# Optimization experiments

Hardware: AMD Instinct MI355X
Metric: run time of the kernel (lower is better)

The kernel has to match this reference:

```python
import jax, jax.numpy as jnp
import numpy as np

TEMPERATURE = 0.3


def setup_inputs() -> dict:
    key = jax.random.key(0)
    k1, k2, k3 = jax.random.split(key, 3)
    B, C = 65536, 1000
    logits = jax.random.normal(k1, (B, C), dtype=jnp.float32)
    targets = jax.random.randint(k2, (B,), 0, C, dtype=jnp.int64)
    similarity_matrix = jax.random.uniform(k3, (C, C), dtype=jnp.float32)
    return {"logits": logits, "targets": targets, "similarity_matrix": similarity_matrix}


def reference(logits, targets, similarity_matrix):
    # Gather per-sample similarity rows: [B, C]
    sim_rows = similarity_matrix[targets]
    # soft_targets = normalized exp(-sim/T) == softmax(-sim/T) along classes
    soft_targets = jax.nn.softmax(-sim_rows / TEMPERATURE, axis=1)
    log_probs = jax.nn.log_softmax(logits, axis=1)
    loss = -(soft_targets * log_probs).sum(axis=1).mean()
    return loss
```

## Files before the change

### kernel.cpp

```cpp
#include <hip/hip_runtime.h>
#include <math.h>


#define TEMPERATURE 0.3f
#define C_DIM 1000
#define LOSS_BLOCKS 2048

typedef float f4 __attribute__((ext_vector_type(4)));

__device__ __forceinline__ float waveAllSum(float v) {
    #pragma unroll
    for (int m = 1; m < 64; m <<= 1) v += __shfl_xor(v, m, 64);
    return v;
}

__global__ void soft_targets_kernel(const float* __restrict__ sim,
                                    float* __restrict__ P) {
    const int wid  = threadIdx.x >> 6;
    const int lane = threadIdx.x & 63;
    const int c = blockIdx.x * 4 + wid;

    const f4* row  = (const f4*)(sim + (size_t)c * C_DIM);
    f4*       prow = (f4*)(P + (size_t)c * C_DIM);

    const bool tail = lane < 58;
    const int  i3   = tail ? lane + 192 : lane;

    f4 v0 = row[lane];
    f4 v1 = row[lane + 64];
    f4 v2 = row[lane + 128];
    f4 v3 = row[i3];

    const float s = -1.0f / TEMPERATURE;
    f4 e0, e1, e2, e3;
    e0.x = __expf(v0.x * s); e0.y = __expf(v0.y * s); e0.z = __expf(v0.z * s); e0.w = __expf(v0.w * s);
    e1.x = __expf(v1.x * s); e1.y = __expf(v1.y * s); e1.z = __expf(v1.z * s); e1.w = __expf(v1.w * s);
    e2.x = __expf(v2.x * s); e2.y = __expf(v2.y * s); e2.z = __expf(v2.z * s); e2.w = __expf(v2.w * s);
    e3.x = __expf(v3.x * s); e3.y = __expf(v3.y * s); e3.z = __expf(v3.z * s); e3.w = __expf(v3.w * s);

    float sum = (e0.x + e0.y + e0.z + e0.w)
              + (e1.x + e1.y + e1.z + e1.w)
              + (e2.x + e2.y + e2.z + e2.w)
              + (tail ? (e3.x + e3.y + e3.z + e3.w) : 0.0f);
    sum = waveAllSum(sum);
    const float inv = 1.0f / sum;

    prow[lane]       = e0 * inv;
    prow[lane + 64]  = e1 * inv;
    prow[lane + 128] = e2 * inv;
    if (tail) prow[lane + 192] = e3 * inv;
}

__device__ __forceinline__ void sample_body(const float* __restrict__ logits,
                                            const float* __restrict__ P,
                                            int i, int t, int lane, int i3, bool tail,
                                            float& es_out, float& acc_dt) {
    const f4* lrow = (const f4*)(logits + (size_t)i * C_DIM);
    const f4* prow = (const f4*)(P + (size_t)t * C_DIM);

    f4 a0 = __builtin_nontemporal_load(lrow + lane);
    f4 a1 = __builtin_nontemporal_load(lrow + lane + 64);
    f4 a2 = __builtin_nontemporal_load(lrow + lane + 128);
    f4 a3 = __builtin_nontemporal_load(lrow + i3);
    f4 p0 = prow[lane];
    f4 p1 = prow[lane + 64];
    f4 p2 = prow[lane + 128];
    f4 p3 = prow[i3];

    float es = (__expf(a0.x) + __expf(a0.y) + __expf(a0.z) + __expf(a0.w))
             + (__expf(a1.x) + __expf(a1.y) + __expf(a1.z) + __expf(a1.w))
             + (__expf(a2.x) + __expf(a2.y) + __expf(a2.z) + __expf(a2.w));
    float es3 = __expf(a3.x) + __expf(a3.y) + __expf(a3.z) + __expf(a3.w);

    float dt = a0.x * p0.x + a0.y * p0.y + a0.z * p0.z + a0.w * p0.w
             + a1.x * p1.x + a1.y * p1.y + a1.z * p1.z + a1.w * p1.w
             + a2.x * p2.x + a2.y * p2.y + a2.z * p2.z + a2.w * p2.w;
    float dt3 = a3.x * p3.x + a3.y * p3.y + a3.z * p3.z + a3.w * p3.w;

    if (tail) { es += es3; dt += dt3; }
    es_out = es;
    acc_dt += dt;
}

__global__ void loss_kernel(const float* __restrict__ logits,
                            const int* __restrict__ targets,
                            const float* __restrict__ P,
                            float* __restrict__ out,
                            float invB, int B) {
    const int wid  = threadIdx.x >> 6;
    const int lane = threadIdx.x & 63;
    const int wave   = blockIdx.x * 4 + wid;
    const int nwaves = gridDim.x * 4;

    const bool tail = lane < 58;
    const int  i3   = tail ? lane + 192 : lane;

    float acc_log = 0.0f;
    float acc_dt  = 0.0f;

    int i = wave;
    for (; i + nwaves < B; i += 2 * nwaves) {
        const int ta = targets[i];
        const int tb = targets[i + nwaves];
        float esA, esB;
        sample_body(logits, P, i,          ta, lane, i3, tail, esA, acc_dt);
        sample_body(logits, P, i + nwaves, tb, lane, i3, tail, esB, acc_dt);
        esA = waveAllSum(esA);
        esB = waveAllSum(esB);
        acc_log += __logf(esA) + __logf(esB);
    }
    for (; i < B; i += nwaves) {
        const int t = targets[i];
        float es;
        sample_body(logits, P, i, t, lane, i3, tail, es, acc_dt);
        es = waveAllSum(es);
        acc_log += __logf(es);
    }

    const float dt_total = waveAllSum(acc_dt);
    __shared__ float sloc[4];
    if (lane == 0) sloc[wid] = acc_log - dt_total;
    __syncthreads();
    if (threadIdx.x == 0) {
        const float blk = sloc[0] + sloc[1] + sloc[2] + sloc[3];
        atomicAdd(out, blk * invB);
    }
}

extern "C" void kernel_launch(void* const* d_in, const int* in_sizes, int n_in,
                              void* d_out, int out_size, void* d_ws, size_t ws_size,
                              hipStream_t stream) {
    const float* logits  = (const float*)d_in[0];
    const int*   targets = (const int*)d_in[1];
    const float* sim     = (const float*)d_in[2];
    float* out = (float*)d_out;
    float* P   = (float*)d_ws;

    const int B = in_sizes[1];

    hipMemsetAsync(out, 0, sizeof(float), stream);
    soft_targets_kernel<<<250, 256, 0, stream>>>(sim, P);
    loss_kernel<<<LOSS_BLOCKS, 256, 0, stream>>>(logits, targets, P, out,
                                                 1.0f / (float)B, B);
}
```

Before: 350.6 us.

## Software-pipeline loss loop with double-buffered loads and drop memset launch

Restructures the loss kernel loop to process chunks of 8 samples per wave, with their target indices prefetched. Each sample's logits and soft-target row loads are issued one sample ahead into a double buffer, so memory latency overlaps with the exp/dot computation. The output zeroing moves from a separate hipMemsetAsync into the soft-targets kernel, removing one launch. The extra in-flight registers may lower occupancy.

```diff
diff --git a/kernel.cpp b/kernel.cpp
--- a/kernel.cpp
+++ b/kernel.cpp
@@ -5,6 +5,7 @@
 #define TEMPERATURE 0.3f
 #define C_DIM 1000
 #define LOSS_BLOCKS 2048
+#define CHUNK 8
 
 typedef float f4 __attribute__((ext_vector_type(4)));
 
@@ -15,7 +16,10 @@
 }
 
 __global__ void soft_targets_kernel(const float* __restrict__ sim,
-                                    float* __restrict__ P) {
+                                    float* __restrict__ P,
+                                    float* __restrict__ out) {
+    if (blockIdx.x == 0 && threadIdx.x == 0) out[0] = 0.0f;
+
     const int wid  = threadIdx.x >> 6;
     const int lane = threadIdx.x & 63;
     const int c = blockIdx.x * 4 + wid;
@@ -51,42 +55,45 @@
     if (tail) prow[lane + 192] = e3 * inv;
 }
 
-__device__ __forceinline__ void sample_body(const float* __restrict__ logits,
+__device__ __forceinline__ void issue_loads(const float* __restrict__ logits,
                                             const float* __restrict__ P,
-                                            int i, int t, int lane, int i3, bool tail,
-                                            float& es_out, float& acc_dt) {
+                                            int i, int t, int lane, int i3,
+                                            f4* A, f4* Pp) {
     const f4* lrow = (const f4*)(logits + (size_t)i * C_DIM);
     const f4* prow = (const f4*)(P + (size_t)t * C_DIM);
+    A[0]  = __builtin_nontemporal_load(lrow + lane);
+    A[1]  = __builtin_nontemporal_load(lrow + lane + 64);
+    A[2]  = __builtin_nontemporal_load(lrow + lane + 128);
+    A[3]  = __builtin_nontemporal_load(lrow + i3);
+    Pp[0] = prow[lane];
+    Pp[1] = prow[lane + 64];
+    Pp[2] = prow[lane + 128];
+    Pp[3] = prow[i3];
+}
 
-    f4 a0 = __builtin_nontemporal_load(lrow + lane);
-    f4 a1 = __builtin_nontemporal_load(lrow + lane + 64);
-    f4 a2 = __builtin_nontemporal_load(lrow + lane + 128);
-    f4 a3 = __builtin_nontemporal_load(lrow + i3);
-    f4 p0 = prow[lane];
-    f4 p1 = prow[lane + 64];
-    f4 p2 = prow[lane + 128];
-    f4 p3 = prow[i3];
+__device__ __forceinline__ void compute_sample(const f4* A, const f4* Pp, bool tail,
+                                               float& es_out, float& acc_dt) {
+    float es = (__expf(A[0].x) + __expf(A[0].y) + __expf(A[0].z) + __expf(A[0].w))
+             + (__expf(A[1].x) + __expf(A[1].y) + __expf(A[1].z) + __expf(A[1].w))
+             + (__expf(A[2].x) + __expf(A[2].y) + __expf(A[2].z) + __expf(A[2].w));
+    float es3 = __expf(A[3].x) + __expf(A[3].y) + __expf(A[3].z) + __expf(A[3].w);
 
-    float es = (__expf(a0.x) + __expf(a0.y) + __expf(a0.z) + __expf(a0.w))
-             + (__expf(a1.x) + __expf(a1.y) + __expf(a1.z) + __expf(a1.w))
-             + (__expf(a2.x) + __expf(a2.y) + __expf(a2.z) + __expf(a2.w));
-    float es3 = __expf(a3.x) + __expf(a3.y) + __expf(a3.z) + __expf(a3.w);
-
-    float dt = a0.x * p0.x + a0.y * p0.y + a0.z * p0.z + a0.w * p0.w
-             + a1.x * p1.x + a1.y * p1.y + a1.z * p1.z + a1.w * p1.w
-             + a2.x * p2.x + a2.y * p2.y + a2.z * p2.z + a2.w * p2.w;
-    float dt3 = a3.x * p3.x + a3.y * p3.y + a3.z * p3.z + a3.w * p3.w;
+    float dt = A[0].x * Pp[0].x + A[0].y * Pp[0].y + A[0].z * Pp[0].z + A[0].w * Pp[0].w
+             + A[1].x * Pp[1].x + A[1].y * Pp[1].y + A[1].z * Pp[1].z + A[1].w * Pp[1].w
+             + A[2].x * Pp[2].x + A[2].y * Pp[2].y + A[2].z * Pp[2].z + A[2].w * Pp[2].w;
+    float dt3 = A[3].x * Pp[3].x + A[3].y * Pp[3].y + A[3].z * Pp[3].z + A[3].w * Pp[3].w;
 
     if (tail) { es += es3; dt += dt3; }
     es_out = es;
     acc_dt += dt;
 }
 
-__global__ void loss_kernel(const float* __restrict__ logits,
-                            const int* __restrict__ targets,
-                            const float* __restrict__ P,
-                            float* __restrict__ out,
-                            float invB, int B) {
+__global__ void __launch_bounds__(256)
+loss_kernel(const float* __restrict__ logits,
+            const int* __restrict__ targets,
+            const float* __restrict__ P,
+            float* __restrict__ out,
+            float invB, int B) {
     const int wid  = threadIdx.x >> 6;
     const int lane = threadIdx.x & 63;
     const int wave   = blockIdx.x * 4 + wid;
@@ -98,21 +105,35 @@
     float acc_log = 0.0f;
     float acc_dt  = 0.0f;
 
-    int i = wave;
-    for (; i + nwaves < B; i += 2 * nwaves) {
-        const int ta = targets[i];
-        const int tb = targets[i + nwaves];
-        float esA, esB;
-        sample_body(logits, P, i,          ta, lane, i3, tail, esA, acc_dt);
-        sample_body(logits, P, i + nwaves, tb, lane, i3, tail, esB, acc_dt);
-        esA = waveAllSum(esA);
-        esB = waveAllSum(esB);
-        acc_log += __logf(esA) + __logf(esB);
+    const int chunk_stride = CHUNK * nwaves;
+    int base = wave;
+
+    for (; base + chunk_stride - nwaves < B; base += chunk_stride) {
+        int t[CHUNK];
+        #pragma unroll
+        for (int k = 0; k < CHUNK; k++) t[k] = targets[base + k * nwaves];
+
+        f4 A[2][4], Pp[2][4];
+        issue_loads(logits, P, base, t[0], lane, i3, A[0], Pp[0]);
+
+        #pragma unroll
+        for (int k = 0; k < CHUNK; k++) {
+            if (k + 1 < CHUNK) {
+                issue_loads(logits, P, base + (k + 1) * nwaves, t[k + 1],
+                            lane, i3, A[(k + 1) & 1], Pp[(k + 1) & 1]);
+            }
+            float es;
+            compute_sample(A[k & 1], Pp[k & 1], tail, es, acc_dt);
+            es = waveAllSum(es);
+            acc_log += __logf(es);
+        }
     }
-    for (; i < B; i += nwaves) {
+    for (int i = base; i < B; i += nwaves) {
         const int t = targets[i];
+        f4 A[4], Pp[4];
+        issue_loads(logits, P, i, t, lane, i3, A, Pp);
         float es;
-        sample_body(logits, P, i, t, lane, i3, tail, es, acc_dt);
+        compute_sample(A, Pp, tail, es, acc_dt);
         es = waveAllSum(es);
         acc_log += __logf(es);
     }
@@ -138,8 +159,7 @@
 
     const int B = in_sizes[1];
 
-    hipMemsetAsync(out, 0, sizeof(float), stream);
-    soft_targets_kernel<<<250, 256, 0, stream>>>(sim, P);
+    soft_targets_kernel<<<250, 256, 0, stream>>>(sim, P, out);
     loss_kernel<<<LOSS_BLOCKS, 256, 0, stream>>>(logits, targets, P, out,
                                                  1.0f / (float)B, B);
 }
```

Result: faster. 340.8 us (-2.8%).
